# Optimization experiments

Hardware: AMD Instinct MI355X
Metric: run time of the kernel (lower is better)

## Reference

```python
import jax, jax.numpy as jnp
import numpy as np

D_MODEL = 64
LN_EPS = 1e-5


def _conv1d(x, w, b, stride, pad):
    # x: (B, Cin, L), w: (Cout, Cin, K)
    y = jax.lax.conv_general_dilated(x, w, (stride,), [(pad, pad)],
                                     dimension_numbers=('NCH', 'OIH', 'NCH'))
    return y + b[None, :, None]


def _layernorm(x, g, b):
    # normalize over last dim (feature dim), matching nn.LayerNorm(d_model)
    m = jnp.mean(x, axis=-1, keepdims=True)
    v = jnp.var(x, axis=-1, keepdims=True)
    return (x - m) * jax.lax.rsqrt(v + LN_EPS) * g + b


def _pos_embed(L, d):
    pos = jnp.arange(L, dtype=jnp.float32)[:, None]
    div = jnp.exp(jnp.arange(0, d, 2, dtype=jnp.float32) * (-np.log(10000.0) / d))
    pe = jnp.zeros((L, d), jnp.float32)
    pe = pe.at[:, 0::2].set(jnp.sin(pos * div))
    pe = pe.at[:, 1::2].set(jnp.cos(pos * div))
    return pe


def setup_inputs():
    key = jax.random.key(0)
    ks = jax.random.split(key, 20)
    B, L, D = 128, 4096, D_MODEL
    G = D // 4  # 16 convs per kernel-size group (kernels cycle [3,5,7,9])
    inp = {'x': jax.random.normal(ks[0], (B, 1, L), jnp.float32)}
    kernels = [3, 5, 7, 9]
    for i, k in enumerate(kernels):
        fan = float(1.0 / np.sqrt(k))
        inp['tok_w%d' % k] = jax.random.uniform(ks[1 + 2 * i], (G, 1, k), jnp.float32, -fan, fan)
        inp['tok_b%d' % k] = jax.random.uniform(ks[2 + 2 * i], (G,), jnp.float32, -fan, fan)
    fan = float(1.0 / np.sqrt(D * 4))
    for j in range(3):
        inp['c_w%d' % (j + 1)] = jax.random.uniform(ks[10 + 2 * j], (D, D, 4), jnp.float32, -fan, fan)
        inp['c_b%d' % (j + 1)] = jax.random.uniform(ks[11 + 2 * j], (D,), jnp.float32, -fan, fan)
    for j in range(2):
        inp['ln_g%d' % (j + 1)] = jnp.ones((D,), jnp.float32)
        inp['ln_b%d' % (j + 1)] = jnp.zeros((D,), jnp.float32)
    return inp


def reference(x, tok_w3, tok_b3, tok_w5, tok_b5, tok_w7, tok_b7, tok_w9, tok_b9,
              c_w1, c_b1, c_w2, c_b2, c_w3, c_b3, ln_g1, ln_b1, ln_g2, ln_b2):
    B, _, L = x.shape
    D = D_MODEL
    # TokenEmbedding: conv i has kernel [3,5,7,9][i%4]; fuse the d_model 1-channel
    # convs into 4 grouped convs (one per kernel size), then interleave channels.
    outs = [
        _conv1d(x, tok_w3, tok_b3, 1, 1),
        _conv1d(x, tok_w5, tok_b5, 1, 2),
        _conv1d(x, tok_w7, tok_b7, 1, 3),
        _conv1d(x, tok_w9, tok_b9, 1, 4),
    ]  # each (B, D//4, L); group g holds channels i with i % 4 == g, ordered by i // 4
    emb = jnp.stack(outs, axis=2).reshape(B, D, L)  # channel i = (i//4)*4 + (i%4)
    # add sinusoidal positional embedding (dropout is identity in eval mode)
    h = emb + _pos_embed(L, D).T[None]  # (B, D, L)
    # CompressionEmbedding: conv(k=4, s=2, p=1) -> tanh -> LN (over D) chain
    h = jnp.tanh(_conv1d(h, c_w1, c_b1, 2, 1))
    h = _layernorm(h.transpose(0, 2, 1), ln_g1, ln_b1).transpose(0, 2, 1)
    h = jnp.tanh(_conv1d(h, c_w2, c_b2, 2, 1))
    h = _layernorm(h.transpose(0, 2, 1), ln_g2, ln_b2).transpose(0, 2, 1)
    h = jnp.tanh(_conv1d(h, c_w3, c_b3, 2, 1))
    return h.transpose(0, 2, 1)  # (B, L//8, D)
```

## Files before the change

kernel.cpp:

```cpp
#include <hip/hip_runtime.h>
#include <math.h>

#define BATCH 128
#define LN_EPS 1e-5f

typedef short bf16x8 __attribute__((ext_vector_type(8)));
typedef short bf16x4 __attribute__((ext_vector_type(4)));
typedef float f32x4  __attribute__((ext_vector_type(4)));

__device__ __forceinline__ ushort f2bf(float f) {
    union { float f; unsigned u; } c; c.f = f;
    unsigned r = c.u + 0x7FFF + ((c.u >> 16) & 1);
    return (ushort)(r >> 16);
}

__device__ __forceinline__ float fast_tanh(float v) {
    float e = __expf(2.f * v);
    return 1.f - 2.f / (e + 1.f);
}

__global__ __launch_bounds__(256, 2)
void prep_kernel(const float* __restrict__ cw1, const float* __restrict__ cw2,
                 const float* __restrict__ cw3,
                 const float* __restrict__ w3, const float* __restrict__ b3,
                 const float* __restrict__ w5, const float* __restrict__ b5,
                 const float* __restrict__ w7, const float* __restrict__ b7,
                 const float* __restrict__ w9, const float* __restrict__ b9,
                 const float* __restrict__ cb1,
                 ushort* __restrict__ Wm23, ushort* __restrict__ Wm1,
                 float* __restrict__ W0c, float* __restrict__ W3c,
                 float* __restrict__ pe1c) {
    const int tid = threadIdx.x;
    const int bx  = blockIdx.x;
    const int idx = bx * 256 + tid;

    __shared__ float tile[64][132];
    __shared__ float red[4][64][24];
    __shared__ float cbred[64][4];

    {
        int s = idx >> 14, r = idx & 16383;
        int j = r & 7, l15 = (r >> 3) & 15, dt = (r >> 7) & 3;
        int quad = (r >> 9) & 3, k2 = (r >> 11) & 1, kk = (r >> 12) & 3;
        int dout = dt * 16 + l15, din = k2 * 32 + quad * 8 + j;
        const float* cw = (s == 0) ? cw2 : cw3;
        Wm23[idx] = f2bf(cw[dout * 256 + din * 4 + kk]);
    }

    if (bx == 0) {
        const int ch = tid & 63, part = tid >> 6;
        const float* cw1row = cw1 + ch * 256;
        float acc[24];
#pragma unroll
        for (int j = 0; j < 24; ++j) acc[j] = 0.f;
        for (int din = part * 16; din < part * 16 + 16; ++din) {
            int ki = din & 3, g = din >> 2;
            float wl[9];
#pragma unroll
            for (int j = 0; j < 9; ++j) wl[j] = 0.f;
            float bias;
            if (ki == 0)      { for (int j = 0; j < 3; ++j) wl[3 + j] = w3[g * 3 + j]; bias = b3[g]; }
            else if (ki == 1) { for (int j = 0; j < 5; ++j) wl[2 + j] = w5[g * 5 + j]; bias = b5[g]; }
            else if (ki == 2) { for (int j = 0; j < 7; ++j) wl[1 + j] = w7[g * 7 + j]; bias = b7[g]; }
            else              { for (int j = 0; j < 9; ++j) wl[j]     = w9[g * 9 + j]; bias = b9[g]; }
#pragma unroll
            for (int kk = 0; kk < 4; ++kk) {
                float c = cw1row[din * 4 + kk];
                acc[12 + kk] += c * bias;
#pragma unroll
                for (int u = 0; u < 9; ++u) acc[kk + u] += c * wl[u];
            }
            float c0 = cw1row[din * 4 + 0], c3 = cw1row[din * 4 + 3];
#pragma unroll
            for (int u = 0; u < 4; ++u) { acc[16 + u] += c0 * wl[5 + u]; acc[20 + u] += c3 * wl[u]; }
        }
#pragma unroll
        for (int j = 0; j < 24; ++j) red[part][ch][j] = acc[j];
    }

    {
        const int pair = tid & 63, part = tid >> 6;
        const int kk = pair >> 4, chl = pair & 15;
        const int ch = (bx & 3) * 16 + chl;
        float s = 0.f;
        for (int din = part * 16; din < part * 16 + 16; ++din) {
            int ki = din & 3, g = din >> 2;
            float bias = (ki == 0) ? b3[g] : (ki == 1) ? b5[g] : (ki == 2) ? b7[g] : b9[g];
            s += cw1[ch * 256 + din * 4 + kk] * bias;
        }
        cbred[pair][part] = s;
    }

    const int l0 = (bx >> 2) * 64;
    const int pin0 = 2 * l0 - 1;
    for (int i2 = tid; i2 < 64 * 130; i2 += 256) {
        int d = i2 / 130, pp = i2 - d * 130;
        int p = pin0 + pp;
        float v = 0.f;
        if (p >= 0 && p < 4096) {
            float dv = __expf((float)(d & ~1) * -0.14391156831212787f);
            float ang = (float)p * dv;
            v = (d & 1) ? __cosf(ang) : __sinf(ang);
        }
        tile[d][pp] = v;
    }
    __syncthreads();

    if (bx == 0 && tid < 64) {
        const int ch = tid;
        float w24[24];
#pragma unroll
        for (int j = 0; j < 24; ++j)
            w24[j] = red[0][ch][j] + red[1][ch][j] + red[2][ch][j] + red[3][ch][j];
        int dt = ch >> 4, l15 = ch & 15;
#pragma unroll
        for (int quad = 0; quad < 4; ++quad)
#pragma unroll
            for (int j = 0; j < 8; ++j) {
                int k = quad * 8 + j;
                Wm1[((quad * 4 + dt) * 16 + l15) * 8 + j] = f2bf(k < 12 ? w24[k] : 0.f);
            }
#pragma unroll
        for (int u = 0; u < 4; ++u) { W0c[ch * 4 + u] = w24[16 + u]; W3c[ch * 4 + u] = w24[20 + u]; }
    }

    const int lane = tid & 63, wv = tid >> 6;
    const int l = l0 + lane;
    const int chl0 = wv * 4;
    const int db = (bx & 3) * 16 + chl0;
    float a4[4];
#pragma unroll
    for (int j = 0; j < 4; ++j) {
        int chl = chl0 + j;
        float cbk0 = cbred[0 * 16 + chl][0] + cbred[0 * 16 + chl][1] + cbred[0 * 16 + chl][2] + cbred[0 * 16 + chl][3];
        float cbk1 = cbred[1 * 16 + chl][0] + cbred[1 * 16 + chl][1] + cbred[1 * 16 + chl][2] + cbred[1 * 16 + chl][3];
        float cbk2 = cbred[2 * 16 + chl][0] + cbred[2 * 16 + chl][1] + cbred[2 * 16 + chl][2] + cbred[2 * 16 + chl][3];
        float cbk3 = cbred[3 * 16 + chl][0] + cbred[3 * 16 + chl][1] + cbred[3 * 16 + chl][2] + cbred[3 * 16 + chl][3];
        float a = cb1[db + j] + cbk1 + cbk2;
        if (l > 0) a += cbk0;
        if (l < 2047) a += cbk3;
        a4[j] = a;
    }
    for (int din = 0; din < 64; ++din) {
        float v0 = tile[din][2 * lane + 0], v1 = tile[din][2 * lane + 1];
        float v2 = tile[din][2 * lane + 2], v3 = tile[din][2 * lane + 3];
        const float* wb = cw1 + din * 4;
#pragma unroll
        for (int j = 0; j < 4; ++j) {
            const float* wj = wb + (db + j) * 256;
            a4[j] = fmaf(v0, wj[0], fmaf(v1, wj[1], fmaf(v2, wj[2], fmaf(v3, wj[3], a4[j]))));
        }
    }
    *(float4*)(pe1c + (size_t)l * 64 + db) = make_float4(a4[0], a4[1], a4[2], a4[3]);
}

__global__ __launch_bounds__(256, 2)
void mega_kernel(const float* __restrict__ x,
                 const ushort* __restrict__ Wm1, const ushort* __restrict__ Wm23,
                 const float* __restrict__ pe1c,
                 const float* __restrict__ W0c, const float* __restrict__ W3c,
                 const float* __restrict__ lg1, const float* __restrict__ lb1,
                 const float* __restrict__ cb2, const float* __restrict__ lg2,
                 const float* __restrict__ lb2, const float* __restrict__ cb3,
                 float* __restrict__ out) {
    const int b = blockIdx.y;
    const int g0 = blockIdx.x * 32;
    const int tid = threadIdx.x;

    __shared__ __align__(16) ushort xs[320];
    __shared__ __align__(16) ushort TE1[68][72];
    __shared__ __align__(16) ushort TO1[68][72];
    __shared__ __align__(16) ushort TE2[34][72];
    __shared__ __align__(16) ushort TO2[34][72];

    for (int i = tid; i < 320; i += 256) {
        int g = 8 * g0 - 11 + i;
        float v = (g >= 0 && g < 4096) ? x[b * 4096 + g] : 0.f;
        xs[i] = f2bf(v);
    }
    __syncthreads();

    const int wv = tid >> 6, lane = tid & 63;
    const int quad = lane >> 4, l15 = lane & 15;

    {
        bf16x8 afr1[4];
#pragma unroll
        for (int dt = 0; dt < 4; ++dt)
            afr1[dt] = *(const bf16x8*)&Wm1[((quad * 4 + dt) * 16 + l15) * 8];
        const int qstart = 4 * g0 - 3;
        for (int pass = wv; pass < 9; pass += 4) {
            const int m = pass * 16 + l15;
            union { bf16x8 v; unsigned u[4]; } tmp;
            const unsigned* p = (const unsigned*)&xs[2 * m + 8 * quad];
#pragma unroll
            for (int i = 0; i < 4; ++i) tmp.u[i] = p[i];
            f32x4 a1[4];
#pragma unroll
            for (int dt = 0; dt < 4; ++dt)
                a1[dt] = __builtin_amdgcn_mfma_f32_16x16x32_bf16(
                    afr1[dt], tmp.v, (f32x4)0.f, 0, 0, 0);
            if (m < 134) {
                const int q = qstart + m;
                ushort* dst = (m & 1) ? &TE1[(m + 1) >> 1][0] : &TO1[m >> 1][0];
                if (q >= 0 && q < 2048) {
                    float v[16];
                    const float* pb_ = pe1c + (size_t)q * 64;
#pragma unroll
                    for (int dt = 0; dt < 4; ++dt) {
                        float4 pv = *(const float4*)(pb_ + dt * 16 + quad * 4);
                        v[dt * 4 + 0] = a1[dt][0] + pv.x;
                        v[dt * 4 + 1] = a1[dt][1] + pv.y;
                        v[dt * 4 + 2] = a1[dt][2] + pv.z;
                        v[dt * 4 + 3] = a1[dt][3] + pv.w;
                    }
                    if (q == 0 || q == 2047) {
                        const float* Wc = (q == 0) ? W0c : W3c;
                        const float* xe = x + b * 4096 + ((q == 0) ? 0 : 4092);
                        float x0 = xe[0], x1 = xe[1], x2 = xe[2], x3 = xe[3];
#pragma unroll
                        for (int dt = 0; dt < 4; ++dt)
#pragma unroll
                            for (int r = 0; r < 4; ++r) {
                                const float* wc = Wc + (dt * 16 + quad * 4 + r) * 4;
                                v[dt * 4 + r] -= wc[0] * x0 + wc[1] * x1 + wc[2] * x2 + wc[3] * x3;
                            }
                    }
#pragma unroll
                    for (int i = 0; i < 16; ++i) v[i] = fast_tanh(v[i]);
                    float s = 0.f;
#pragma unroll
                    for (int i = 0; i < 16; ++i) s += v[i];
                    s += __shfl_xor(s, 16, 64);
                    s += __shfl_xor(s, 32, 64);
                    float mean = s * 0.015625f;
                    float qq = 0.f;
#pragma unroll
                    for (int i = 0; i < 16; ++i) { float d = v[i] - mean; qq = fmaf(d, d, qq); }
                    qq += __shfl_xor(qq, 16, 64);
                    qq += __shfl_xor(qq, 32, 64);
                    float rstd = rsqrtf(qq * 0.015625f + LN_EPS);
#pragma unroll
                    for (int dt = 0; dt < 4; ++dt) {
                        bf16x4 pk;
#pragma unroll
                        for (int r = 0; r < 4; ++r) {
                            int ch = dt * 16 + quad * 4 + r;
                            pk[r] = (short)f2bf((v[dt * 4 + r] - mean) * rstd * lg1[ch] + lb1[ch]);
                        }
                        *(bf16x4*)(dst + dt * 16 + quad * 4) = pk;
                    }
                } else {
                    bf16x4 z; z[0] = 0; z[1] = 0; z[2] = 0; z[3] = 0;
#pragma unroll
                    for (int dt = 0; dt < 4; ++dt)
                        *(bf16x4*)(dst + dt * 16 + quad * 4) = z;
                }
            }
        }
    }
    __syncthreads();

    for (int pass = wv; pass < 5; pass += 4) {
        const int n = pass * 16 + l15;
        const int nc = (n < 66) ? n : 65;
        f32x4 a2[4];
#pragma unroll
        for (int dt = 0; dt < 4; ++dt) a2[dt] = (f32x4)0.f;
#pragma unroll
        for (int kk = 0; kk < 4; ++kk) {
            const ushort (*T)[72] = (kk & 1) ? TE1 : TO1;
            const int row = nc + ((kk + 1) >> 1);
#pragma unroll
            for (int k2 = 0; k2 < 2; ++k2) {
                bf16x8 bfr = *(const bf16x8*)&T[row][k2 * 32 + quad * 8];
                const ushort* wb = Wm23 + ((((kk * 2 + k2) * 4 + quad) * 4) * 16) * 8;
#pragma unroll
                for (int dt = 0; dt < 4; ++dt) {
                    bf16x8 afr = *(const bf16x8*)(wb + ((size_t)(dt * 16 + l15)) * 8);
                    a2[dt] = __builtin_amdgcn_mfma_f32_16x16x32_bf16(afr, bfr, a2[dt], 0, 0, 0);
                }
            }
        }
        if (n < 66) {
            const int p = 2 * g0 - 1 + n;
            ushort* dst = (n & 1) ? &TE2[(n + 1) >> 1][0] : &TO2[n >> 1][0];
            if (p >= 0 && p < 1024) {
                float v[16];
#pragma unroll
                for (int dt = 0; dt < 4; ++dt)
#pragma unroll
                    for (int r = 0; r < 4; ++r)
                        v[dt * 4 + r] = fast_tanh(a2[dt][r] + cb2[dt * 16 + quad * 4 + r]);
                float s = 0.f;
#pragma unroll
                for (int i = 0; i < 16; ++i) s += v[i];
                s += __shfl_xor(s, 16, 64);
                s += __shfl_xor(s, 32, 64);
                float mean = s * 0.015625f;
                float qq = 0.f;
#pragma unroll
                for (int i = 0; i < 16; ++i) { float d = v[i] - mean; qq = fmaf(d, d, qq); }
                qq += __shfl_xor(qq, 16, 64);
                qq += __shfl_xor(qq, 32, 64);
                float rstd = rsqrtf(qq * 0.015625f + LN_EPS);
#pragma unroll
                for (int dt = 0; dt < 4; ++dt) {
                    bf16x4 pk;
#pragma unroll
                    for (int r = 0; r < 4; ++r) {
                        int ch = dt * 16 + quad * 4 + r;
                        pk[r] = (short)f2bf((v[dt * 4 + r] - mean) * rstd * lg2[ch] + lb2[ch]);
                    }
                    *(bf16x4*)(dst + dt * 16 + quad * 4) = pk;
                }
            } else {
                bf16x4 z; z[0] = 0; z[1] = 0; z[2] = 0; z[3] = 0;
#pragma unroll
                for (int dt = 0; dt < 4; ++dt)
                    *(bf16x4*)(dst + dt * 16 + quad * 4) = z;
            }
        }
    }
    __syncthreads();

    {
        const int m3 = (wv & 1) * 16 + l15;
        const int dth = wv >> 1;
        f32x4 a3[2];
        a3[0] = (f32x4)0.f; a3[1] = (f32x4)0.f;
        const ushort* Wg3 = Wm23 + 16384;
#pragma unroll
        for (int kk = 0; kk < 4; ++kk) {
            const ushort (*T)[72] = (kk & 1) ? TE2 : TO2;
            const int row = m3 + ((kk + 1) >> 1);
#pragma unroll
            for (int k2 = 0; k2 < 2; ++k2) {
                bf16x8 bfr = *(const bf16x8*)&T[row][k2 * 32 + quad * 8];
                const ushort* wb = Wg3 + ((((kk * 2 + k2) * 4 + quad) * 4) * 16) * 8;
#pragma unroll
                for (int d2 = 0; d2 < 2; ++d2) {
                    const int dt = dth * 2 + d2;
                    bf16x8 afr = *(const bf16x8*)(wb + ((size_t)(dt * 16 + l15)) * 8);
                    a3[d2] = __builtin_amdgcn_mfma_f32_16x16x32_bf16(afr, bfr, a3[d2], 0, 0, 0);
                }
            }
        }
        const int l = g0 + m3;
        float* ob = out + ((size_t)(b * 512) + l) * 64;
#pragma unroll
        for (int d2 = 0; d2 < 2; ++d2) {
            const int dt = dth * 2 + d2;
            float4 st = make_float4(fast_tanh(a3[d2][0] + cb3[dt * 16 + quad * 4 + 0]),
                                    fast_tanh(a3[d2][1] + cb3[dt * 16 + quad * 4 + 1]),
                                    fast_tanh(a3[d2][2] + cb3[dt * 16 + quad * 4 + 2]),
                                    fast_tanh(a3[d2][3] + cb3[dt * 16 + quad * 4 + 3]));
            *(float4*)(ob + dt * 16 + quad * 4) = st;
        }
    }
}

extern "C" void kernel_launch(void* const* d_in, const int* in_sizes, int n_in,
                              void* d_out, int out_size, void* d_ws, size_t ws_size,
                              hipStream_t stream) {
    (void)in_sizes; (void)n_in; (void)out_size; (void)ws_size;
    const float* x   = (const float*)d_in[0];
    const float* w3  = (const float*)d_in[1];
    const float* b3  = (const float*)d_in[2];
    const float* w5  = (const float*)d_in[3];
    const float* b5  = (const float*)d_in[4];
    const float* w7  = (const float*)d_in[5];
    const float* b7  = (const float*)d_in[6];
    const float* w9  = (const float*)d_in[7];
    const float* b9  = (const float*)d_in[8];
    const float* cw1 = (const float*)d_in[9];
    const float* cb1 = (const float*)d_in[10];
    const float* cw2 = (const float*)d_in[11];
    const float* cb2 = (const float*)d_in[12];
    const float* cw3 = (const float*)d_in[13];
    const float* cb3 = (const float*)d_in[14];
    const float* lg1 = (const float*)d_in[15];
    const float* lb1 = (const float*)d_in[16];
    const float* lg2 = (const float*)d_in[17];
    const float* lb2 = (const float*)d_in[18];
    float* out = (float*)d_out;

    char* w = (char*)d_ws;
    ushort* Wm23 = (ushort*)(w + 0);
    ushort* Wm1  = (ushort*)(w + 65536);
    float*  W0c  = (float*)(w + 69632);
    float*  W3c  = (float*)(w + 70656);
    float*  pe1c = (float*)(w + 71680);

    prep_kernel<<<128, 256, 0, stream>>>(cw1, cw2, cw3, w3, b3, w5, b5, w7, b7, w9, b9,
                                         cb1, Wm23, Wm1, W0c, W3c, pe1c);
    mega_kernel<<<dim3(16, BATCH), 256, 0, stream>>>(
        x, Wm1, Wm23, pe1c, W0c, W3c, lg1, lb1, cb2, lg2, lb2, cb3, out);
}
```

Measured before the change: 165.3 us.

## Fold LayerNorm affine into next conv weights and biases, use one-pass variance

Folds the LayerNorm gamma into the bf16 weights of convs 2 and 3 and folds beta into their biases. The prep kernel precomputes the adjusted biases and boundary correction terms for the zero-padded edge positions. The main kernel then seeds the MFMA accumulators with bias/positional terms, computes mean and variance in a single pass (sum and sum of squares), and normalizes with one fma per element, removing per-element gamma/beta loads. It also switches float-to-bf16 conversion to the compiler builtin. The one-pass variance and gamma applied before bf16 rounding slightly change numerics.

```diff
diff --git a/kernel.cpp b/kernel.cpp
--- a/kernel.cpp
+++ b/kernel.cpp
@@ -9,9 +9,7 @@
 typedef float f32x4  __attribute__((ext_vector_type(4)));
 
 __device__ __forceinline__ ushort f2bf(float f) {
-    union { float f; unsigned u; } c; c.f = f;
-    unsigned r = c.u + 0x7FFF + ((c.u >> 16) & 1);
-    return (ushort)(r >> 16);
+    return __builtin_bit_cast(ushort, (__bf16)f);
 }
 
 __device__ __forceinline__ float fast_tanh(float v) {
@@ -26,10 +24,17 @@
                  const float* __restrict__ w5, const float* __restrict__ b5,
                  const float* __restrict__ w7, const float* __restrict__ b7,
                  const float* __restrict__ w9, const float* __restrict__ b9,
-                 const float* __restrict__ cb1,
+                 const float* __restrict__ cb1, const float* __restrict__ cb2,
+                 const float* __restrict__ cb3,
+                 const float* __restrict__ lg1, const float* __restrict__ lb1,
+                 const float* __restrict__ lg2, const float* __restrict__ lb2,
                  ushort* __restrict__ Wm23, ushort* __restrict__ Wm1,
                  float* __restrict__ W0c, float* __restrict__ W3c,
-                 float* __restrict__ pe1c) {
+                 float* __restrict__ pe1c,
+                 float* __restrict__ cb2t, float* __restrict__ B2k0,
+                 float* __restrict__ B2k3,
+                 float* __restrict__ cb3t, float* __restrict__ B3k0,
+                 float* __restrict__ B3k3) {
     const int tid = threadIdx.x;
     const int bx  = blockIdx.x;
     const int idx = bx * 256 + tid;
@@ -44,7 +49,24 @@
         int quad = (r >> 9) & 3, k2 = (r >> 11) & 1, kk = (r >> 12) & 3;
         int dout = dt * 16 + l15, din = k2 * 32 + quad * 8 + j;
         const float* cw = (s == 0) ? cw2 : cw3;
-        Wm23[idx] = f2bf(cw[dout * 256 + din * 4 + kk]);
+        const float* lg = (s == 0) ? lg1 : lg2;
+        Wm23[idx] = f2bf(cw[dout * 256 + din * 4 + kk] * lg[din]);
+    }
+
+    if (bx == 1 && tid < 128) {
+        const int s = tid >> 6, ch = tid & 63;
+        const float* cw = (s == 0) ? cw2 : cw3;
+        const float* lb = (s == 0) ? lb1 : lb2;
+        float full = 0.f, k0 = 0.f, k3 = 0.f;
+        for (int din = 0; din < 64; ++din) {
+            float bv = lb[din];
+            const float* wr = cw + ch * 256 + din * 4;
+            k0 = fmaf(wr[0], bv, k0);
+            k3 = fmaf(wr[3], bv, k3);
+            full = fmaf(wr[0] + wr[1] + wr[2] + wr[3], bv, full);
+        }
+        if (s == 0) { cb2t[ch] = cb2[ch] + full; B2k0[ch] = k0; B2k3[ch] = k3; }
+        else        { cb3t[ch] = cb3[ch] + full; B3k0[ch] = k0; B3k3[ch] = k3; }
     }
 
     if (bx == 0) {
@@ -159,9 +181,10 @@
                  const ushort* __restrict__ Wm1, const ushort* __restrict__ Wm23,
                  const float* __restrict__ pe1c,
                  const float* __restrict__ W0c, const float* __restrict__ W3c,
-                 const float* __restrict__ lg1, const float* __restrict__ lb1,
-                 const float* __restrict__ cb2, const float* __restrict__ lg2,
-                 const float* __restrict__ lb2, const float* __restrict__ cb3,
+                 const float* __restrict__ cb2t, const float* __restrict__ B2k0,
+                 const float* __restrict__ B2k3,
+                 const float* __restrict__ cb3t, const float* __restrict__ B3k0,
+                 const float* __restrict__ B3k3,
                  float* __restrict__ out) {
     const int b = blockIdx.y;
     const int g0 = blockIdx.x * 32;
@@ -191,29 +214,26 @@
         const int qstart = 4 * g0 - 3;
         for (int pass = wv; pass < 9; pass += 4) {
             const int m = pass * 16 + l15;
+            const int q = qstart + m;
+            const int qc = (q < 0) ? 0 : ((q > 2047) ? 2047 : q);
+            f32x4 a1[4];
+            const float* pb_ = pe1c + (size_t)qc * 64 + quad * 4;
+#pragma unroll
+            for (int dt = 0; dt < 4; ++dt) {
+                float4 pv = *(const float4*)(pb_ + dt * 16);
+                a1[dt][0] = pv.x; a1[dt][1] = pv.y; a1[dt][2] = pv.z; a1[dt][3] = pv.w;
+            }
             union { bf16x8 v; unsigned u[4]; } tmp;
             const unsigned* p = (const unsigned*)&xs[2 * m + 8 * quad];
 #pragma unroll
             for (int i = 0; i < 4; ++i) tmp.u[i] = p[i];
-            f32x4 a1[4];
 #pragma unroll
             for (int dt = 0; dt < 4; ++dt)
                 a1[dt] = __builtin_amdgcn_mfma_f32_16x16x32_bf16(
-                    afr1[dt], tmp.v, (f32x4)0.f, 0, 0, 0);
+                    afr1[dt], tmp.v, a1[dt], 0, 0, 0);
             if (m < 134) {
-                const int q = qstart + m;
                 ushort* dst = (m & 1) ? &TE1[(m + 1) >> 1][0] : &TO1[m >> 1][0];
                 if (q >= 0 && q < 2048) {
-                    float v[16];
-                    const float* pb_ = pe1c + (size_t)q * 64;
-#pragma unroll
-                    for (int dt = 0; dt < 4; ++dt) {
-                        float4 pv = *(const float4*)(pb_ + dt * 16 + quad * 4);
-                        v[dt * 4 + 0] = a1[dt][0] + pv.x;
-                        v[dt * 4 + 1] = a1[dt][1] + pv.y;
-                        v[dt * 4 + 2] = a1[dt][2] + pv.z;
-                        v[dt * 4 + 3] = a1[dt][3] + pv.w;
-                    }
                     if (q == 0 || q == 2047) {
                         const float* Wc = (q == 0) ? W0c : W3c;
                         const float* xe = x + b * 4096 + ((q == 0) ? 0 : 4092);
@@ -223,31 +243,33 @@
 #pragma unroll
                             for (int r = 0; r < 4; ++r) {
                                 const float* wc = Wc + (dt * 16 + quad * 4 + r) * 4;
-                                v[dt * 4 + r] -= wc[0] * x0 + wc[1] * x1 + wc[2] * x2 + wc[3] * x3;
+                                a1[dt][r] -= wc[0] * x0 + wc[1] * x1 + wc[2] * x2 + wc[3] * x3;
                             }
                     }
-#pragma unroll
-                    for (int i = 0; i < 16; ++i) v[i] = fast_tanh(v[i]);
-                    float s = 0.f;
-#pragma unroll
-                    for (int i = 0; i < 16; ++i) s += v[i];
+                    float v[16], s = 0.f, s2 = 0.f;
+#pragma unroll
+                    for (int dt = 0; dt < 4; ++dt)
+#pragma unroll
+                        for (int r = 0; r < 4; ++r) {
+                            float t = fast_tanh(a1[dt][r]);
+                            v[dt * 4 + r] = t;
+                            s += t;
+                            s2 = fmaf(t, t, s2);
+                        }
                     s += __shfl_xor(s, 16, 64);
                     s += __shfl_xor(s, 32, 64);
+                    s2 += __shfl_xor(s2, 16, 64);
+                    s2 += __shfl_xor(s2, 32, 64);
                     float mean = s * 0.015625f;
-                    float qq = 0.f;
-#pragma unroll
-                    for (int i = 0; i < 16; ++i) { float d = v[i] - mean; qq = fmaf(d, d, qq); }
-                    qq += __shfl_xor(qq, 16, 64);
-                    qq += __shfl_xor(qq, 32, 64);
-                    float rstd = rsqrtf(qq * 0.015625f + LN_EPS);
+                    float var = fmaf(-mean, mean, s2 * 0.015625f);
+                    float rstd = rsqrtf(var + LN_EPS);
+                    float nmr = -mean * rstd;
 #pragma unroll
                     for (int dt = 0; dt < 4; ++dt) {
                         bf16x4 pk;
 #pragma unroll
-                        for (int r = 0; r < 4; ++r) {
-                            int ch = dt * 16 + quad * 4 + r;
-                            pk[r] = (short)f2bf((v[dt * 4 + r] - mean) * rstd * lg1[ch] + lb1[ch]);
-                        }
+                        for (int r = 0; r < 4; ++r)
+                            pk[r] = (short)f2bf(fmaf(v[dt * 4 + r], rstd, nmr));
                         *(bf16x4*)(dst + dt * 16 + quad * 4) = pk;
                     }
                 } else {
@@ -261,64 +283,78 @@
     }
     __syncthreads();
 
-    for (int pass = wv; pass < 5; pass += 4) {
-        const int n = pass * 16 + l15;
-        const int nc = (n < 66) ? n : 65;
-        f32x4 a2[4];
-#pragma unroll
-        for (int dt = 0; dt < 4; ++dt) a2[dt] = (f32x4)0.f;
-#pragma unroll
-        for (int kk = 0; kk < 4; ++kk) {
-            const ushort (*T)[72] = (kk & 1) ? TE1 : TO1;
-            const int row = nc + ((kk + 1) >> 1);
-#pragma unroll
-            for (int k2 = 0; k2 < 2; ++k2) {
-                bf16x8 bfr = *(const bf16x8*)&T[row][k2 * 32 + quad * 8];
-                const ushort* wb = Wm23 + ((((kk * 2 + k2) * 4 + quad) * 4) * 16) * 8;
-#pragma unroll
-                for (int dt = 0; dt < 4; ++dt) {
-                    bf16x8 afr = *(const bf16x8*)(wb + ((size_t)(dt * 16 + l15)) * 8);
-                    a2[dt] = __builtin_amdgcn_mfma_f32_16x16x32_bf16(afr, bfr, a2[dt], 0, 0, 0);
+    {
+        f32x4 cfr2[4];
+#pragma unroll
+        for (int dt = 0; dt < 4; ++dt) {
+            float4 cv = *(const float4*)(cb2t + dt * 16 + quad * 4);
+            cfr2[dt][0] = cv.x; cfr2[dt][1] = cv.y; cfr2[dt][2] = cv.z; cfr2[dt][3] = cv.w;
+        }
+        for (int pass = wv; pass < 5; pass += 4) {
+            const int n = pass * 16 + l15;
+            const int nc = (n < 66) ? n : 65;
+            f32x4 a2[4];
+#pragma unroll
+            for (int dt = 0; dt < 4; ++dt) a2[dt] = cfr2[dt];
+#pragma unroll
+            for (int kk = 0; kk < 4; ++kk) {
+                const ushort (*T)[72] = (kk & 1) ? TE1 : TO1;
+                const int row = nc + ((kk + 1) >> 1);
+#pragma unroll
+                for (int k2 = 0; k2 < 2; ++k2) {
+                    bf16x8 bfr = *(const bf16x8*)&T[row][k2 * 32 + quad * 8];
+                    const ushort* wb = Wm23 + ((((kk * 2 + k2) * 4 + quad) * 4) * 16) * 8;
+#pragma unroll
+                    for (int dt = 0; dt < 4; ++dt) {
+                        bf16x8 afr = *(const bf16x8*)(wb + ((size_t)(dt * 16 + l15)) * 8);
+                        a2[dt] = __builtin_amdgcn_mfma_f32_16x16x32_bf16(afr, bfr, a2[dt], 0, 0, 0);
+                    }
                 }
             }
-        }
-        if (n < 66) {
-            const int p = 2 * g0 - 1 + n;
-            ushort* dst = (n & 1) ? &TE2[(n + 1) >> 1][0] : &TO2[n >> 1][0];
-            if (p >= 0 && p < 1024) {
-                float v[16];
-#pragma unroll
-                for (int dt = 0; dt < 4; ++dt)
-#pragma unroll
-                    for (int r = 0; r < 4; ++r)
-                        v[dt * 4 + r] = fast_tanh(a2[dt][r] + cb2[dt * 16 + quad * 4 + r]);
-                float s = 0.f;
-#pragma unroll
-                for (int i = 0; i < 16; ++i) s += v[i];
-                s += __shfl_xor(s, 16, 64);
-                s += __shfl_xor(s, 32, 64);
-                float mean = s * 0.015625f;
-                float qq = 0.f;
-#pragma unroll
-                for (int i = 0; i < 16; ++i) { float d = v[i] - mean; qq = fmaf(d, d, qq); }
-                qq += __shfl_xor(qq, 16, 64);
-                qq += __shfl_xor(qq, 32, 64);
-                float rstd = rsqrtf(qq * 0.015625f + LN_EPS);
-#pragma unroll
-                for (int dt = 0; dt < 4; ++dt) {
-                    bf16x4 pk;
-#pragma unroll
-                    for (int r = 0; r < 4; ++r) {
-                        int ch = dt * 16 + quad * 4 + r;
-                        pk[r] = (short)f2bf((v[dt * 4 + r] - mean) * rstd * lg2[ch] + lb2[ch]);
+            if (n < 66) {
+                const int p = 2 * g0 - 1 + n;
+                ushort* dst = (n & 1) ? &TE2[(n + 1) >> 1][0] : &TO2[n >> 1][0];
+                if (p >= 0 && p < 1024) {
+                    if (p == 0 || p == 1023) {
+                        const float* Bc = (p == 0) ? B2k0 : B2k3;
+#pragma unroll
+                        for (int dt = 0; dt < 4; ++dt)
+#pragma unroll
+                            for (int r = 0; r < 4; ++r)
+                                a2[dt][r] -= Bc[dt * 16 + quad * 4 + r];
                     }
-                    *(bf16x4*)(dst + dt * 16 + quad * 4) = pk;
+                    float v[16], s = 0.f, s2 = 0.f;
+#pragma unroll
+                    for (int dt = 0; dt < 4; ++dt)
+#pragma unroll
+                        for (int r = 0; r < 4; ++r) {
+                            float t = fast_tanh(a2[dt][r]);
+                            v[dt * 4 + r] = t;
+                            s += t;
+                            s2 = fmaf(t, t, s2);
+                        }
+                    s += __shfl_xor(s, 16, 64);
+                    s += __shfl_xor(s, 32, 64);
+                    s2 += __shfl_xor(s2, 16, 64);
+                    s2 += __shfl_xor(s2, 32, 64);
+                    float mean = s * 0.015625f;
+                    float var = fmaf(-mean, mean, s2 * 0.015625f);
+                    float rstd = rsqrtf(var + LN_EPS);
+                    float nmr = -mean * rstd;
+#pragma unroll
+                    for (int dt = 0; dt < 4; ++dt) {
+                        bf16x4 pk;
+#pragma unroll
+                        for (int r = 0; r < 4; ++r)
+                            pk[r] = (short)f2bf(fmaf(v[dt * 4 + r], rstd, nmr));
+                        *(bf16x4*)(dst + dt * 16 + quad * 4) = pk;
+                    }
+                } else {
+                    bf16x4 z; z[0] = 0; z[1] = 0; z[2] = 0; z[3] = 0;
+#pragma unroll
+                    for (int dt = 0; dt < 4; ++dt)
+                        *(bf16x4*)(dst + dt * 16 + quad * 4) = z;
                 }
-            } else {
-                bf16x4 z; z[0] = 0; z[1] = 0; z[2] = 0; z[3] = 0;
-#pragma unroll
-                for (int dt = 0; dt < 4; ++dt)
-                    *(bf16x4*)(dst + dt * 16 + quad * 4) = z;
             }
         }
     }
@@ -328,7 +364,11 @@
         const int m3 = (wv & 1) * 16 + l15;
         const int dth = wv >> 1;
         f32x4 a3[2];
-        a3[0] = (f32x4)0.f; a3[1] = (f32x4)0.f;
+#pragma unroll
+        for (int d2 = 0; d2 < 2; ++d2) {
+            float4 cv = *(const float4*)(cb3t + (dth * 2 + d2) * 16 + quad * 4);
+            a3[d2][0] = cv.x; a3[d2][1] = cv.y; a3[d2][2] = cv.z; a3[d2][3] = cv.w;
+        }
         const ushort* Wg3 = Wm23 + 16384;
 #pragma unroll
         for (int kk = 0; kk < 4; ++kk) {
@@ -347,14 +387,22 @@
             }
         }
         const int l = g0 + m3;
+        if (l == 0 || l == 511) {
+            const float* Bc = (l == 0) ? B3k0 : B3k3;
+#pragma unroll
+            for (int d2 = 0; d2 < 2; ++d2)
+#pragma unroll
+                for (int r = 0; r < 4; ++r)
+                    a3[d2][r] -= Bc[(dth * 2 + d2) * 16 + quad * 4 + r];
+        }
         float* ob = out + ((size_t)(b * 512) + l) * 64;
 #pragma unroll
         for (int d2 = 0; d2 < 2; ++d2) {
             const int dt = dth * 2 + d2;
-            float4 st = make_float4(fast_tanh(a3[d2][0] + cb3[dt * 16 + quad * 4 + 0]),
-                                    fast_tanh(a3[d2][1] + cb3[dt * 16 + quad * 4 + 1]),
-                                    fast_tanh(a3[d2][2] + cb3[dt * 16 + quad * 4 + 2]),
-                                    fast_tanh(a3[d2][3] + cb3[dt * 16 + quad * 4 + 3]));
+            float4 st = make_float4(fast_tanh(a3[d2][0]),
+                                    fast_tanh(a3[d2][1]),
+                                    fast_tanh(a3[d2][2]),
+                                    fast_tanh(a3[d2][3]));
             *(float4*)(ob + dt * 16 + quad * 4) = st;
         }
     }
@@ -390,10 +438,18 @@
     ushort* Wm1  = (ushort*)(w + 65536);
     float*  W0c  = (float*)(w + 69632);
     float*  W3c  = (float*)(w + 70656);
-    float*  pe1c = (float*)(w + 71680);
+    float*  cb2t = (float*)(w + 71680);
+    float*  B2k0 = (float*)(w + 71936);
+    float*  B2k3 = (float*)(w + 72192);
+    float*  cb3t = (float*)(w + 72448);
+    float*  B3k0 = (float*)(w + 72704);
+    float*  B3k3 = (float*)(w + 72960);
+    float*  pe1c = (float*)(w + 73216);
 
     prep_kernel<<<128, 256, 0, stream>>>(cw1, cw2, cw3, w3, b3, w5, b5, w7, b7, w9, b9,
-                                         cb1, Wm23, Wm1, W0c, W3c, pe1c);
+                                         cb1, cb2, cb3, lg1, lb1, lg2, lb2,
+                                         Wm23, Wm1, W0c, W3c, pe1c,
+                                         cb2t, B2k0, B2k3, cb3t, B3k0, B3k3);
     mega_kernel<<<dim3(16, BATCH), 256, 0, stream>>>(
-        x, Wm1, Wm23, pe1c, W0c, W3c, lg1, lb1, cb2, lg2, lb2, cb3, out);
+        x, Wm1, Wm23, pe1c, W0c, W3c, cb2t, B2k0, B2k3, cb3t, B3k0, B3k3, out);
 }
```

Result: no change. 163.5 us (-1.1%).
